# Kernel optimization log

Measured on AMD Instinct MI355X. Metric: run time of the kernel, lower is better.

The kernel has to match this reference:

```python
import jax, jax.numpy as jnp
import numpy as np


def _gcn_conv(x, edge_index, W, b):
    # PyG GCNConv: h = x @ W; out = D^{-1/2}(A+I)D^{-1/2} h + b
    N = x.shape[0]
    src, dst = edge_index[0], edge_index[1]
    # degree with self-loops (edge weights = 1)
    deg = jax.ops.segment_sum(jnp.ones(src.shape[0], x.dtype), dst, num_segments=N) + 1.0
    dis = jax.lax.rsqrt(deg)  # deg >= 1 so finite
    h = x @ W  # [N, F_out]
    norm = dis[src] * dis[dst]  # [E]
    msg = h[src] * norm[:, None]  # [E, F_out] -- dominant memory traffic
    agg = jax.ops.segment_sum(msg, dst, num_segments=N)
    # self-loop contribution: norm_ii = dis_i^2
    out = agg + h * (dis * dis)[:, None] + b
    return out


def setup_inputs() -> dict:
    key = jax.random.key(0)
    k1, k2, k3, k4, k5, k6 = jax.random.split(key, 6)
    N, E = 100000, 1600000
    in_ch, hid, out_ch = 256, 128, 64  # hid = 2*out_channels
    x = jax.random.normal(k1, (N, in_ch), dtype=jnp.float32)
    edge_index = jax.random.randint(k2, (2, E), 0, N, dtype=jnp.int64)
    # Glorot-style init for GCN weights, zero bias (PyG default)
    W1 = jax.random.normal(k3, (in_ch, hid), dtype=jnp.float32) / np.sqrt(in_ch)
    b1 = jnp.zeros((hid,), jnp.float32)
    W2 = jax.random.normal(k4, (hid, out_ch), dtype=jnp.float32) / np.sqrt(hid)
    b2 = jnp.zeros((out_ch,), jnp.float32)
    return {"x": x, "edge_index": edge_index, "W1": W1, "b1": b1, "W2": W2, "b2": b2}


def reference(x, edge_index, W1, b1, W2, b2):
    # Encoder.forward: k=2 layers of activation(GCNConv(x, edge_index))
    h = jax.nn.relu(_gcn_conv(x, edge_index, W1, b1))
    h = jax.nn.relu(_gcn_conv(h, edge_index, W2, b2))
    return h
```

## Files before the change

kernel.cpp:

```cpp
#include <hip/hip_runtime.h>
#include <math.h>

#define THREADS 256

static inline int cdiv(long long a, long long b) { return (int)((a + b - 1) / b); }

typedef __attribute__((ext_vector_type(8))) short bf16x8;
typedef __attribute__((ext_vector_type(4))) float f32x4;

__device__ inline unsigned f2bf_rne_u(float f) {
    unsigned u = __builtin_bit_cast(unsigned, f);
    return (u + 0x7FFFu + ((u >> 16) & 1u)) >> 16;
}
__device__ inline float bfu2f(unsigned h) {
    unsigned u = h << 16;
    return __builtin_bit_cast(float, u);
}


__global__ __launch_bounds__(THREADS)
void hist_rank_kernel(const int* __restrict__ dst, int* __restrict__ deg,
                      int* __restrict__ rank, int E) {
    int i = blockIdx.x * blockDim.x + threadIdx.x;
    if (i < E) rank[i] = atomicAdd(&deg[dst[i]], 1);
}


#define SCAN_BLOCK 256
#define SCAN_ITEMS 4

__global__ __launch_bounds__(SCAN_BLOCK)
void scan_block_kernel(const int* __restrict__ in, int* __restrict__ out,
                       int* __restrict__ blockSums, float* __restrict__ dis, int n) {
    __shared__ int sdata[SCAN_BLOCK];
    int base = blockIdx.x * (SCAN_BLOCK * SCAN_ITEMS);
    int tid = threadIdx.x;
    int v[SCAN_ITEMS];
    int sum = 0;
    #pragma unroll
    for (int k = 0; k < SCAN_ITEMS; ++k) {
        int idx = base + tid * SCAN_ITEMS + k;
        v[k] = (idx < n) ? in[idx] : 0;
        if (idx < n) dis[idx] = rsqrtf((float)v[k] + 1.0f);
        sum += v[k];
    }
    sdata[tid] = sum;
    __syncthreads();
    for (int off = 1; off < SCAN_BLOCK; off <<= 1) {
        int t = (tid >= off) ? sdata[tid - off] : 0;
        __syncthreads();
        sdata[tid] += t;
        __syncthreads();
    }
    if (tid == SCAN_BLOCK - 1) blockSums[blockIdx.x] = sdata[SCAN_BLOCK - 1];
    int run = (tid == 0) ? 0 : sdata[tid - 1];
    #pragma unroll
    for (int k = 0; k < SCAN_ITEMS; ++k) {
        int idx = base + tid * SCAN_ITEMS + k;
        if (idx < n) out[idx] = run;
        run += v[k];
    }
}

__global__ __launch_bounds__(SCAN_BLOCK)
void scan_sums_kernel(int* __restrict__ blockSums, int nB) {
    __shared__ int sdata[SCAN_BLOCK];
    int tid = threadIdx.x;
    sdata[tid] = (tid < nB) ? blockSums[tid] : 0;
    __syncthreads();
    for (int off = 1; off < SCAN_BLOCK; off <<= 1) {
        int t = (tid >= off) ? sdata[tid - off] : 0;
        __syncthreads();
        sdata[tid] += t;
        __syncthreads();
    }
    int excl = (tid == 0) ? 0 : sdata[tid - 1];
    if (tid < nB) blockSums[tid] = excl;
}

__global__ __launch_bounds__(SCAN_BLOCK)
void scan_add_kernel(int* __restrict__ out, const int* __restrict__ blockSums,
                     int n, int E) {
    int base = blockIdx.x * (SCAN_BLOCK * SCAN_ITEMS);
    int add = blockSums[blockIdx.x];
    #pragma unroll
    for (int k = 0; k < SCAN_ITEMS; ++k) {
        int idx = base + threadIdx.x * SCAN_ITEMS + k;
        if (idx < n) out[idx] += add;
    }
    if (blockIdx.x == 0 && threadIdx.x == 0) out[n] = E;
}


__global__ __launch_bounds__(THREADS)
void fill_col_rank_kernel(const int* __restrict__ src, const int* __restrict__ dst,
                          const int* __restrict__ rank, const int* __restrict__ rowptr,
                          int* __restrict__ col, int E) {
    int base = (blockIdx.x * blockDim.x + threadIdx.x) * 4;
    if (base + 3 < E) {
        int4 d = *(const int4*)(dst + base);
        int4 r = *(const int4*)(rank + base);
        int4 s = *(const int4*)(src + base);
        col[rowptr[d.x] + r.x] = s.x;
        col[rowptr[d.y] + r.y] = s.y;
        col[rowptr[d.z] + r.z] = s.z;
        col[rowptr[d.w] + r.w] = s.w;
    } else {
        for (int e = base; e < E; ++e)
            col[rowptr[dst[e]] + rank[e]] = src[e];
    }
}


template<int F, int VEC>
__global__ __launch_bounds__(THREADS)
void gather_bf16_kernel(const unsigned short* __restrict__ g, const int* __restrict__ col,
                        const int* __restrict__ rowptr, const float* __restrict__ dis,
                        const float* __restrict__ bias, float* __restrict__ out, int N) {
    int wid = (int)((blockIdx.x * (long long)blockDim.x + threadIdx.x) >> 6);
    wid = __builtin_amdgcn_readfirstlane(wid);
    const int lane = threadIdx.x & 63;
    if (wid >= N) return;
    const float di = dis[wid];
    const int loff = lane * VEC;

    float acc0 = 0.0f, acc1 = 0.0f;

    auto loadrow = [&](int s) -> unsigned {
        const unsigned short* p = g + (size_t)s * F + loff;
        if (VEC == 2) return *(const unsigned*)p;
        else return (unsigned)*p;
    };
    auto addconv = [&](unsigned u) {
        if (VEC == 2) {
            acc0 += bfu2f(u & 0xFFFFu);
            acc1 += __builtin_bit_cast(float, u & 0xFFFF0000u);
        } else {
            acc0 += bfu2f(u);
        }
    };

    addconv(loadrow(wid));

    int start = __builtin_amdgcn_readfirstlane(rowptr[wid]);
    int end   = __builtin_amdgcn_readfirstlane(rowptr[wid + 1]);
    const int* c = col + start;
    int rem = end - start;

    if (rem >= 4) {
        int s0 = __builtin_amdgcn_readfirstlane(c[0]);
        int s1 = __builtin_amdgcn_readfirstlane(c[1]);
        int s2 = __builtin_amdgcn_readfirstlane(c[2]);
        int s3 = __builtin_amdgcn_readfirstlane(c[3]);
        unsigned u0 = loadrow(s0), u1 = loadrow(s1), u2 = loadrow(s2), u3 = loadrow(s3);
        c += 4; rem -= 4;
        while (rem >= 4) {
            int t0 = __builtin_amdgcn_readfirstlane(c[0]);
            int t1 = __builtin_amdgcn_readfirstlane(c[1]);
            int t2 = __builtin_amdgcn_readfirstlane(c[2]);
            int t3 = __builtin_amdgcn_readfirstlane(c[3]);
            unsigned v0 = loadrow(t0), v1 = loadrow(t1), v2 = loadrow(t2), v3 = loadrow(t3);
            addconv(u0); addconv(u1); addconv(u2); addconv(u3);
            u0 = v0; u1 = v1; u2 = v2; u3 = v3;
            c += 4; rem -= 4;
        }
        addconv(u0); addconv(u1); addconv(u2); addconv(u3);
    }
    while (rem > 0) {
        int s = __builtin_amdgcn_readfirstlane(c[0]);
        addconv(loadrow(s));
        ++c; --rem;
    }

    float* orow = out + (size_t)wid * F + loff;
    float v0 = di * acc0 + bias[loff];
    if (VEC == 2) {
        float v1 = di * acc1 + bias[loff + 1];
        float2 st = make_float2(fmaxf(v0, 0.0f), fmaxf(v1, 0.0f));
        *(float2*)orow = st;
    } else {
        *orow = fmaxf(v0, 0.0f);
    }
}


__global__ __launch_bounds__(64)
void make_bfrag_both_kernel(const float* __restrict__ W1, short* __restrict__ f1,
                            const float* __restrict__ W2, short* __restrict__ f2) {
    int lane = threadIdx.x;
    int b = blockIdx.x;
    const float* W; short* frag; int NCT, ctks;
    if (b < 64) { W = W1; frag = f1; NCT = 8; ctks = b; }
    else        { W = W2; frag = f2; NCT = 4; ctks = b - 64; }
    int Nn = NCT * 16;
    int ct = ctks % NCT;
    int ks = ctks / NCT;
    int colc = ct * 16 + (lane & 15);
    int kbase = ks * 32 + (lane >> 4) * 8;
    short* base = frag + (size_t)ctks * 1024 + lane * 8;
    #pragma unroll
    for (int j = 0; j < 8; ++j) {
        float v = W[(size_t)(kbase + j) * Nn + colc];
        unsigned h = f2bf_rne_u(v);
        base[j] = (short)h;
        base[512 + j] = (short)f2bf_rne_u(v - bfu2f(h));
    }
}

template<int NCT, int KS>
__global__ __launch_bounds__(THREADS)
void mfma_gemm_bf16out_kernel(const float* __restrict__ A, const short* __restrict__ Bfrag,
                              unsigned short* __restrict__ G, const float* __restrict__ dis,
                              int M) {
    constexpr int K = KS * 32;
    constexpr int Nn = NCT * 16;
    const int lane = threadIdx.x & 63;
    const int wave = threadIdx.x >> 6;
    const int rowBase = blockIdx.x * 128 + wave * 32;
    const int arow0 = rowBase + (lane & 15);
    const int kgrp = (lane >> 4) * 8;

    f32x4 acc[2][NCT] = {};

    for (int ks = 0; ks < KS; ++ks) {
        const int kbase = ks * 32 + kgrp;
        bf16x8 ahi[2], alo[2];
        #pragma unroll
        for (int t = 0; t < 2; ++t) {
            int r = arow0 + t * 16;
            if (r >= M) r = M - 1;
            const float* ap = A + (size_t)r * K + kbase;
            float4 v0 = *(const float4*)ap;
            float4 v1 = *(const float4*)(ap + 4);
            float av[8] = {v0.x, v0.y, v0.z, v0.w, v1.x, v1.y, v1.z, v1.w};
            #pragma unroll
            for (int j = 0; j < 8; ++j) {
                unsigned h = f2bf_rne_u(av[j]);
                ahi[t][j] = (short)h;
                alo[t][j] = (short)f2bf_rne_u(av[j] - bfu2f(h));
            }
        }
        #pragma unroll
        for (int ct = 0; ct < NCT; ++ct) {
            const short* bp = Bfrag + (size_t)(ks * NCT + ct) * 1024 + lane * 8;
            bf16x8 bhi = *(const bf16x8*)bp;
            bf16x8 blo = *(const bf16x8*)(bp + 512);
            #pragma unroll
            for (int t = 0; t < 2; ++t) {
                acc[t][ct] = __builtin_amdgcn_mfma_f32_16x16x32_bf16(ahi[t], bhi, acc[t][ct], 0, 0, 0);
                acc[t][ct] = __builtin_amdgcn_mfma_f32_16x16x32_bf16(ahi[t], blo, acc[t][ct], 0, 0, 0);
                acc[t][ct] = __builtin_amdgcn_mfma_f32_16x16x32_bf16(alo[t], bhi, acc[t][ct], 0, 0, 0);
            }
        }
    }

    const int drow0 = rowBase + (lane >> 4) * 4;
    #pragma unroll
    for (int t = 0; t < 2; ++t) {
        #pragma unroll
        for (int r = 0; r < 4; ++r) {
            int row = drow0 + t * 16 + r;
            if (row < M) {
                float dval = dis[row];
                unsigned short* gp = G + (size_t)row * Nn + (lane & 15);
                #pragma unroll
                for (int ct = 0; ct < NCT; ++ct)
                    gp[ct * 16] = (unsigned short)f2bf_rne_u(acc[t][ct][r] * dval);
            }
        }
    }
}


#define BM 64
#define BN 64
#define BK 16

__global__ __launch_bounds__(THREADS)
void sgemm_kernel(const float* __restrict__ A, const float* __restrict__ B,
                  float* __restrict__ C, int M, int N, int K) {
    __shared__ float As[BK][BM + 1];
    __shared__ float Bs[BK][BN + 1];

    const int tid = threadIdx.x;
    const int tr = tid / 16;
    const int tc = tid % 16;
    const int rowBase = blockIdx.y * BM;
    const int colBase = blockIdx.x * BN;

    float acc[4][4] = {};

    for (int k0 = 0; k0 < K; k0 += BK) {
        #pragma unroll
        for (int i = tid; i < BM * BK; i += THREADS) {
            int r = i / BK, c = i % BK;
            int gr = rowBase + r;
            As[c][r] = (gr < M) ? A[(size_t)gr * K + k0 + c] : 0.0f;
        }
        #pragma unroll
        for (int i = tid; i < BK * BN; i += THREADS) {
            int r = i / BN, c = i % BN;
            Bs[r][c] = B[(size_t)(k0 + r) * N + colBase + c];
        }
        __syncthreads();

        #pragma unroll
        for (int k = 0; k < BK; ++k) {
            float a[4], b[4];
            #pragma unroll
            for (int m = 0; m < 4; ++m) a[m] = As[k][tr * 4 + m];
            #pragma unroll
            for (int n = 0; n < 4; ++n) b[n] = Bs[k][tc * 4 + n];
            #pragma unroll
            for (int m = 0; m < 4; ++m)
                #pragma unroll
                for (int n = 0; n < 4; ++n)
                    acc[m][n] += a[m] * b[n];
        }
        __syncthreads();
    }

    #pragma unroll
    for (int m = 0; m < 4; ++m) {
        int gr = rowBase + tr * 4 + m;
        if (gr >= M) continue;
        #pragma unroll
        for (int n = 0; n < 4; ++n) {
            C[(size_t)gr * N + colBase + tc * 4 + n] = acc[m][n];
        }
    }
}

__global__ __launch_bounds__(THREADS)
void init_agg_kernel(const float* __restrict__ h, const float* __restrict__ dis,
                     float* __restrict__ agg, int N, int F) {
    int i = blockIdx.x * blockDim.x + threadIdx.x;
    int total = N * (F / 4);
    if (i >= total) return;
    int node = i / (F / 4);
    float d = dis[node];
    float w = d * d;
    float4 v = ((const float4*)h)[i];
    v.x *= w; v.y *= w; v.z *= w; v.w *= w;
    ((float4*)agg)[i] = v;
}

__global__ __launch_bounds__(THREADS)
void edge_scatter_kernel(const float* __restrict__ h, const int* __restrict__ src,
                         const int* __restrict__ dst, const float* __restrict__ dis,
                         float* __restrict__ agg, int E, int F) {
    int lanesPerEdge = F / 4;
    int tid = blockIdx.x * blockDim.x + threadIdx.x;
    int e = tid / lanesPerEdge;
    int c = tid % lanesPerEdge;
    if (e >= E) return;
    int s = src[e];
    int d = dst[e];
    float w = dis[s] * dis[d];
    float4 hv = ((const float4*)(h + (size_t)s * F))[c];
    float* ap = agg + (size_t)d * F + (size_t)c * 4;
    atomicAdd(ap + 0, hv.x * w);
    atomicAdd(ap + 1, hv.y * w);
    atomicAdd(ap + 2, hv.z * w);
    atomicAdd(ap + 3, hv.w * w);
}

__global__ __launch_bounds__(THREADS)
void finalize_kernel(const float* __restrict__ agg, const float* __restrict__ b,
                     float* __restrict__ out, int N, int F) {
    int i = blockIdx.x * blockDim.x + threadIdx.x;
    int total = N * (F / 4);
    if (i >= total) return;
    int c4 = i % (F / 4);
    float4 bv = ((const float4*)b)[c4];
    float4 v = ((const float4*)agg)[i];
    v.x = fmaxf(v.x + bv.x, 0.0f);
    v.y = fmaxf(v.y + bv.y, 0.0f);
    v.z = fmaxf(v.z + bv.z, 0.0f);
    v.w = fmaxf(v.w + bv.w, 0.0f);
    ((float4*)out)[i] = v;
}

__global__ __launch_bounds__(THREADS)
void fdeg_kernel(const int* __restrict__ dst, float* __restrict__ deg, int E) {
    int i = blockIdx.x * blockDim.x + threadIdx.x;
    if (i < E) atomicAdd(&deg[dst[i]], 1.0f);
}

__global__ __launch_bounds__(THREADS)
void fdis_kernel(float* __restrict__ deg, int N) {
    int i = blockIdx.x * blockDim.x + threadIdx.x;
    if (i < N) deg[i] = rsqrtf(deg[i] + 1.0f);
}


extern "C" void kernel_launch(void* const* d_in, const int* in_sizes, int n_in,
                              void* d_out, int out_size, void* d_ws, size_t ws_size,
                              hipStream_t stream) {
    const float* x  = (const float*)d_in[0];
    const int*   ei = (const int*)d_in[1];
    const float* W1 = (const float*)d_in[2];
    const float* b1 = (const float*)d_in[3];
    const float* W2 = (const float*)d_in[4];
    const float* b2 = (const float*)d_in[5];

    const int E    = in_sizes[1] / 2;
    const int hid  = in_sizes[3];
    const int outc = in_sizes[5];
    const int inc  = in_sizes[2] / hid;
    const int N    = in_sizes[0] / inc;

    const int* src = ei;
    const int* dst = ei + E;
    float* out = (float*)d_out;
    char* ws = (char*)d_ws;

    auto al = [](size_t v) { return (v + 255) & ~(size_t)255; };
    size_t o_dis  = 0;
    size_t o_deg  = al(o_dis + (size_t)N * 4);
    size_t o_rp   = al(o_deg + (size_t)N * 4);
    size_t o_bs   = al(o_rp + ((size_t)N + 1) * 4);
    size_t o_col  = al(o_bs + 4096);
    size_t o_rank = al(o_col + (size_t)E * 4);
    size_t o_bf1  = al(o_rank + (size_t)E * 4);
    size_t o_bf2  = al(o_bf1 + 131072);
    size_t o_G    = al(o_bf2 + 32768);
    size_t o_B    = al(o_G + (size_t)N * hid * 2);
    size_t need   = o_B + (size_t)N * hid * 4;

    if (ws_size >= need && N <= SCAN_BLOCK * SCAN_BLOCK * SCAN_ITEMS &&
        hid == 128 && outc == 64 && inc == 256) {
        float* dis    = (float*)(ws + o_dis);
        int*   deg    = (int*)(ws + o_deg);
        int*   rowptr = (int*)(ws + o_rp);
        int*   bsums  = (int*)(ws + o_bs);
        int*   col    = (int*)(ws + o_col);
        int*   rank   = (int*)(ws + o_rank);
        short* bf1    = (short*)(ws + o_bf1);
        short* bf2    = (short*)(ws + o_bf2);
        unsigned short* gbuf = (unsigned short*)(ws + o_G);
        float* out1   = (float*)(ws + o_B);

        hipMemsetAsync(deg, 0, (size_t)N * 4, stream);
        hist_rank_kernel<<<cdiv(E, THREADS), THREADS, 0, stream>>>(dst, deg, rank, E);

        int nB = cdiv(N, SCAN_BLOCK * SCAN_ITEMS);
        scan_block_kernel<<<nB, SCAN_BLOCK, 0, stream>>>(deg, rowptr, bsums, dis, N);
        scan_sums_kernel<<<1, SCAN_BLOCK, 0, stream>>>(bsums, nB);
        scan_add_kernel<<<nB, SCAN_BLOCK, 0, stream>>>(rowptr, bsums, N, E);

        fill_col_rank_kernel<<<cdiv(cdiv(E, 4), THREADS), THREADS, 0, stream>>>(
            src, dst, rank, rowptr, col, E);

        make_bfrag_both_kernel<<<80, 64, 0, stream>>>(W1, bf1, W2, bf2);

        mfma_gemm_bf16out_kernel<8, 8><<<cdiv(N, 128), THREADS, 0, stream>>>(x, bf1, gbuf, dis, N);
        gather_bf16_kernel<128, 2><<<cdiv((long long)N * 64, THREADS), THREADS, 0, stream>>>(
            gbuf, col, rowptr, dis, b1, out1, N);

        mfma_gemm_bf16out_kernel<4, 4><<<cdiv(N, 128), THREADS, 0, stream>>>(out1, bf2, gbuf, dis, N);
        gather_bf16_kernel<64, 1><<<cdiv((long long)N * 64, THREADS), THREADS, 0, stream>>>(
            gbuf, col, rowptr, dis, b2, out, N);
        return;
    }

    float* dis = (float*)ws;
    size_t off1 = ((size_t)N * 4 + 255) & ~(size_t)255;
    float* h1 = (float*)(ws + off1);
    size_t off2 = off1 + ((((size_t)N * hid * 4) + 255) & ~(size_t)255);
    float* agg1 = (float*)(ws + off2);
    float* h2   = agg1;
    float* agg2 = agg1 + (size_t)N * outc;

    hipMemsetAsync(dis, 0, (size_t)N * 4, stream);
    fdeg_kernel<<<cdiv(E, THREADS), THREADS, 0, stream>>>(dst, dis, E);
    fdis_kernel<<<cdiv(N, THREADS), THREADS, 0, stream>>>(dis, N);

    {
        dim3 grid(hid / BN, cdiv(N, BM));
        sgemm_kernel<<<grid, THREADS, 0, stream>>>(x, W1, h1, N, hid, inc);
    }
    init_agg_kernel<<<cdiv((long long)N * hid / 4, THREADS), THREADS, 0, stream>>>(h1, dis, agg1, N, hid);
    edge_scatter_kernel<<<cdiv((long long)E * (hid / 4), THREADS), THREADS, 0, stream>>>(
        h1, src, dst, dis, agg1, E, hid);
    finalize_kernel<<<cdiv((long long)N * hid / 4, THREADS), THREADS, 0, stream>>>(agg1, b1, h1, N, hid);

    {
        dim3 grid(outc / BN, cdiv(N, BM));
        sgemm_kernel<<<grid, THREADS, 0, stream>>>(h1, W2, h2, N, outc, hid);
    }
    init_agg_kernel<<<cdiv((long long)N * outc / 4, THREADS), THREADS, 0, stream>>>(h2, dis, agg2, N, outc);
    edge_scatter_kernel<<<cdiv((long long)E * (outc / 4), THREADS), THREADS, 0, stream>>>(
        h2, src, dst, dis, agg2, E, outc);
    finalize_kernel<<<cdiv((long long)N * outc / 4, THREADS), THREADS, 0, stream>>>(agg2, b2, out, N, outc);
}
```

Baseline: 279.3 us.

## Merge independent CSR-build and GEMM launches into combined block-partitioned kernels

Independent stages now share launches, with blocks split by index. The degree histogram runs alongside building the weight fragments, and the CSR column fill runs alongside the first-layer MFMA GEMM. This cuts two kernel launches and lets the scatter-bound fill overlap with the compute-bound GEMM. The histogram now handles four edges per thread using vectorized int4 loads and stores. The risks are uneven block mixes within one grid and the GEMM's register pressure applying to the fill blocks.

```diff
diff --git a/kernel.cpp b/kernel.cpp
--- a/kernel.cpp
+++ b/kernel.cpp
@@ -18,11 +18,155 @@
 }
 
 
-__global__ __launch_bounds__(THREADS)
-void hist_rank_kernel(const int* __restrict__ dst, int* __restrict__ deg,
-                      int* __restrict__ rank, int E) {
-    int i = blockIdx.x * blockDim.x + threadIdx.x;
-    if (i < E) rank[i] = atomicAdd(&deg[dst[i]], 1);
+__device__ __forceinline__ void hist_body(const int* __restrict__ dst, int* __restrict__ deg,
+                                          int* __restrict__ rank, int E, int blk) {
+    int base = (blk * THREADS + (int)threadIdx.x) * 4;
+    if (base + 3 < E) {
+        int4 d = *(const int4*)(dst + base);
+        int4 r;
+        r.x = atomicAdd(&deg[d.x], 1);
+        r.y = atomicAdd(&deg[d.y], 1);
+        r.z = atomicAdd(&deg[d.z], 1);
+        r.w = atomicAdd(&deg[d.w], 1);
+        *(int4*)(rank + base) = r;
+    } else {
+        for (int e = base; e < E; ++e) rank[e] = atomicAdd(&deg[dst[e]], 1);
+    }
+}
+
+__device__ __forceinline__ void bfrag_unit(const float* __restrict__ W, short* __restrict__ frag,
+                                           int NCT, int ctks, int lane) {
+    int Nn = NCT * 16;
+    int ct = ctks % NCT;
+    int ks = ctks / NCT;
+    int colc = ct * 16 + (lane & 15);
+    int kbase = ks * 32 + (lane >> 4) * 8;
+    short* base = frag + (size_t)ctks * 1024 + lane * 8;
+    #pragma unroll
+    for (int j = 0; j < 8; ++j) {
+        float v = W[(size_t)(kbase + j) * Nn + colc];
+        unsigned h = f2bf_rne_u(v);
+        base[j] = (short)h;
+        base[512 + j] = (short)f2bf_rne_u(v - bfu2f(h));
+    }
+}
+
+__device__ __forceinline__ void fill_body(const int* __restrict__ src, const int* __restrict__ dst,
+                                          const int* __restrict__ rank, const int* __restrict__ rowptr,
+                                          int* __restrict__ col, int E, int blk) {
+    int base = (blk * THREADS + (int)threadIdx.x) * 4;
+    if (base + 3 < E) {
+        int4 d = *(const int4*)(dst + base);
+        int4 r = *(const int4*)(rank + base);
+        int4 s = *(const int4*)(src + base);
+        col[rowptr[d.x] + r.x] = s.x;
+        col[rowptr[d.y] + r.y] = s.y;
+        col[rowptr[d.z] + r.z] = s.z;
+        col[rowptr[d.w] + r.w] = s.w;
+    } else {
+        for (int e = base; e < E; ++e)
+            col[rowptr[dst[e]] + rank[e]] = src[e];
+    }
+}
+
+template<int NCT, int KS>
+__device__ __forceinline__ void gemm_body(const float* __restrict__ A, const short* __restrict__ Bfrag,
+                                          unsigned short* __restrict__ G, const float* __restrict__ dis,
+                                          int M, int blk) {
+    constexpr int K = KS * 32;
+    constexpr int Nn = NCT * 16;
+    const int lane = threadIdx.x & 63;
+    const int wave = threadIdx.x >> 6;
+    const int rowBase = blk * 128 + wave * 32;
+    const int arow0 = rowBase + (lane & 15);
+    const int kgrp = (lane >> 4) * 8;
+
+    f32x4 acc[2][NCT] = {};
+
+    for (int ks = 0; ks < KS; ++ks) {
+        const int kbase = ks * 32 + kgrp;
+        bf16x8 ahi[2], alo[2];
+        #pragma unroll
+        for (int t = 0; t < 2; ++t) {
+            int r = arow0 + t * 16;
+            if (r >= M) r = M - 1;
+            const float* ap = A + (size_t)r * K + kbase;
+            float4 v0 = *(const float4*)ap;
+            float4 v1 = *(const float4*)(ap + 4);
+            float av[8] = {v0.x, v0.y, v0.z, v0.w, v1.x, v1.y, v1.z, v1.w};
+            #pragma unroll
+            for (int j = 0; j < 8; ++j) {
+                unsigned h = f2bf_rne_u(av[j]);
+                ahi[t][j] = (short)h;
+                alo[t][j] = (short)f2bf_rne_u(av[j] - bfu2f(h));
+            }
+        }
+        #pragma unroll
+        for (int ct = 0; ct < NCT; ++ct) {
+            const short* bp = Bfrag + (size_t)(ks * NCT + ct) * 1024 + lane * 8;
+            bf16x8 bhi = *(const bf16x8*)bp;
+            bf16x8 blo = *(const bf16x8*)(bp + 512);
+            #pragma unroll
+            for (int t = 0; t < 2; ++t) {
+                acc[t][ct] = __builtin_amdgcn_mfma_f32_16x16x32_bf16(ahi[t], bhi, acc[t][ct], 0, 0, 0);
+                acc[t][ct] = __builtin_amdgcn_mfma_f32_16x16x32_bf16(ahi[t], blo, acc[t][ct], 0, 0, 0);
+                acc[t][ct] = __builtin_amdgcn_mfma_f32_16x16x32_bf16(alo[t], bhi, acc[t][ct], 0, 0, 0);
+            }
+        }
+    }
+
+    const int drow0 = rowBase + (lane >> 4) * 4;
+    #pragma unroll
+    for (int t = 0; t < 2; ++t) {
+        #pragma unroll
+        for (int r = 0; r < 4; ++r) {
+            int row = drow0 + t * 16 + r;
+            if (row < M) {
+                float dval = dis[row];
+                unsigned short* gp = G + (size_t)row * Nn + (lane & 15);
+                #pragma unroll
+                for (int ct = 0; ct < NCT; ++ct)
+                    gp[ct * 16] = (unsigned short)f2bf_rne_u(acc[t][ct][r] * dval);
+            }
+        }
+    }
+}
+
+
+__global__ __launch_bounds__(THREADS)
+void hist_bfrag_kernel(const int* __restrict__ dst, int* __restrict__ deg, int* __restrict__ rank, int E,
+                       const float* __restrict__ W1, short* __restrict__ bf1,
+                       const float* __restrict__ W2, short* __restrict__ bf2, int nbHist) {
+    int b = (int)blockIdx.x;
+    if (b < nbHist) {
+        hist_body(dst, deg, rank, E, b);
+    } else {
+        int u = (b - nbHist) * 4 + ((int)threadIdx.x >> 6);
+        int lane = threadIdx.x & 63;
+        if (u < 64) bfrag_unit(W1, bf1, 8, u, lane);
+        else if (u < 80) bfrag_unit(W2, bf2, 4, u - 64, lane);
+    }
+}
+
+template<int NCT, int KS>
+__global__ __launch_bounds__(THREADS)
+void fill_gemm_kernel(const int* __restrict__ src, const int* __restrict__ dst,
+                      const int* __restrict__ rank, const int* __restrict__ rowptr,
+                      int* __restrict__ col, int E,
+                      const float* __restrict__ A, const short* __restrict__ Bfrag,
+                      unsigned short* __restrict__ G, const float* __restrict__ dis,
+                      int M, int nbFill) {
+    int b = (int)blockIdx.x;
+    if (b < nbFill) fill_body(src, dst, rank, rowptr, col, E, b);
+    else gemm_body<NCT, KS>(A, Bfrag, G, dis, M, b - nbFill);
+}
+
+template<int NCT, int KS>
+__global__ __launch_bounds__(THREADS)
+void mfma_gemm_bf16out_kernel(const float* __restrict__ A, const short* __restrict__ Bfrag,
+                              unsigned short* __restrict__ G, const float* __restrict__ dis,
+                              int M) {
+    gemm_body<NCT, KS>(A, Bfrag, G, dis, M, (int)blockIdx.x);
 }
 
 
@@ -89,26 +233,6 @@
         if (idx < n) out[idx] += add;
     }
     if (blockIdx.x == 0 && threadIdx.x == 0) out[n] = E;
-}
-
-
-__global__ __launch_bounds__(THREADS)
-void fill_col_rank_kernel(const int* __restrict__ src, const int* __restrict__ dst,
-                          const int* __restrict__ rank, const int* __restrict__ rowptr,
-                          int* __restrict__ col, int E) {
-    int base = (blockIdx.x * blockDim.x + threadIdx.x) * 4;
-    if (base + 3 < E) {
-        int4 d = *(const int4*)(dst + base);
-        int4 r = *(const int4*)(rank + base);
-        int4 s = *(const int4*)(src + base);
-        col[rowptr[d.x] + r.x] = s.x;
-        col[rowptr[d.y] + r.y] = s.y;
-        col[rowptr[d.z] + r.z] = s.z;
-        col[rowptr[d.w] + r.w] = s.w;
-    } else {
-        for (int e = base; e < E; ++e)
-            col[rowptr[dst[e]] + rank[e]] = src[e];
-    }
 }
 
 
@@ -180,94 +304,6 @@
         *(float2*)orow = st;
     } else {
         *orow = fmaxf(v0, 0.0f);
-    }
-}
-
-
-__global__ __launch_bounds__(64)
-void make_bfrag_both_kernel(const float* __restrict__ W1, short* __restrict__ f1,
-                            const float* __restrict__ W2, short* __restrict__ f2) {
-    int lane = threadIdx.x;
-    int b = blockIdx.x;
-    const float* W; short* frag; int NCT, ctks;
-    if (b < 64) { W = W1; frag = f1; NCT = 8; ctks = b; }
-    else        { W = W2; frag = f2; NCT = 4; ctks = b - 64; }
-    int Nn = NCT * 16;
-    int ct = ctks % NCT;
-    int ks = ctks / NCT;
-    int colc = ct * 16 + (lane & 15);
-    int kbase = ks * 32 + (lane >> 4) * 8;
-    short* base = frag + (size_t)ctks * 1024 + lane * 8;
-    #pragma unroll
-    for (int j = 0; j < 8; ++j) {
-        float v = W[(size_t)(kbase + j) * Nn + colc];
-        unsigned h = f2bf_rne_u(v);
-        base[j] = (short)h;
-        base[512 + j] = (short)f2bf_rne_u(v - bfu2f(h));
-    }
-}
-
-template<int NCT, int KS>
-__global__ __launch_bounds__(THREADS)
-void mfma_gemm_bf16out_kernel(const float* __restrict__ A, const short* __restrict__ Bfrag,
-                              unsigned short* __restrict__ G, const float* __restrict__ dis,
-                              int M) {
-    constexpr int K = KS * 32;
-    constexpr int Nn = NCT * 16;
-    const int lane = threadIdx.x & 63;
-    const int wave = threadIdx.x >> 6;
-    const int rowBase = blockIdx.x * 128 + wave * 32;
-    const int arow0 = rowBase + (lane & 15);
-    const int kgrp = (lane >> 4) * 8;
-
-    f32x4 acc[2][NCT] = {};
-
-    for (int ks = 0; ks < KS; ++ks) {
-        const int kbase = ks * 32 + kgrp;
-        bf16x8 ahi[2], alo[2];
-        #pragma unroll
-        for (int t = 0; t < 2; ++t) {
-            int r = arow0 + t * 16;
-            if (r >= M) r = M - 1;
-            const float* ap = A + (size_t)r * K + kbase;
-            float4 v0 = *(const float4*)ap;
-            float4 v1 = *(const float4*)(ap + 4);
-            float av[8] = {v0.x, v0.y, v0.z, v0.w, v1.x, v1.y, v1.z, v1.w};
-            #pragma unroll
-            for (int j = 0; j < 8; ++j) {
-                unsigned h = f2bf_rne_u(av[j]);
-                ahi[t][j] = (short)h;
-                alo[t][j] = (short)f2bf_rne_u(av[j] - bfu2f(h));
-            }
-        }
-        #pragma unroll
-        for (int ct = 0; ct < NCT; ++ct) {
-            const short* bp = Bfrag + (size_t)(ks * NCT + ct) * 1024 + lane * 8;
-            bf16x8 bhi = *(const bf16x8*)bp;
-            bf16x8 blo = *(const bf16x8*)(bp + 512);
-            #pragma unroll
-            for (int t = 0; t < 2; ++t) {
-                acc[t][ct] = __builtin_amdgcn_mfma_f32_16x16x32_bf16(ahi[t], bhi, acc[t][ct], 0, 0, 0);
-                acc[t][ct] = __builtin_amdgcn_mfma_f32_16x16x32_bf16(ahi[t], blo, acc[t][ct], 0, 0, 0);
-                acc[t][ct] = __builtin_amdgcn_mfma_f32_16x16x32_bf16(alo[t], bhi, acc[t][ct], 0, 0, 0);
-            }
-        }
-    }
-
-    const int drow0 = rowBase + (lane >> 4) * 4;
-    #pragma unroll
-    for (int t = 0; t < 2; ++t) {
-        #pragma unroll
-        for (int r = 0; r < 4; ++r) {
-            int row = drow0 + t * 16 + r;
-            if (row < M) {
-                float dval = dis[row];
-                unsigned short* gp = G + (size_t)row * Nn + (lane & 15);
-                #pragma unroll
-                for (int ct = 0; ct < NCT; ++ct)
-                    gp[ct * 16] = (unsigned short)f2bf_rne_u(acc[t][ct][r] * dval);
-            }
-        }
     }
 }
 
@@ -441,20 +477,22 @@
         unsigned short* gbuf = (unsigned short*)(ws + o_G);
         float* out1   = (float*)(ws + o_B);
 
+        const int nbHist = cdiv(E, 4 * THREADS);
+        const int nbFill = cdiv(E, 4 * THREADS);
+        const int nbGemm1 = cdiv(N, 128);
+
         hipMemsetAsync(deg, 0, (size_t)N * 4, stream);
-        hist_rank_kernel<<<cdiv(E, THREADS), THREADS, 0, stream>>>(dst, deg, rank, E);
+        hist_bfrag_kernel<<<nbHist + 20, THREADS, 0, stream>>>(
+            dst, deg, rank, E, W1, bf1, W2, bf2, nbHist);
 
         int nB = cdiv(N, SCAN_BLOCK * SCAN_ITEMS);
         scan_block_kernel<<<nB, SCAN_BLOCK, 0, stream>>>(deg, rowptr, bsums, dis, N);
         scan_sums_kernel<<<1, SCAN_BLOCK, 0, stream>>>(bsums, nB);
         scan_add_kernel<<<nB, SCAN_BLOCK, 0, stream>>>(rowptr, bsums, N, E);
 
-        fill_col_rank_kernel<<<cdiv(cdiv(E, 4), THREADS), THREADS, 0, stream>>>(
-            src, dst, rank, rowptr, col, E);
-
-        make_bfrag_both_kernel<<<80, 64, 0, stream>>>(W1, bf1, W2, bf2);
-
-        mfma_gemm_bf16out_kernel<8, 8><<<cdiv(N, 128), THREADS, 0, stream>>>(x, bf1, gbuf, dis, N);
+        fill_gemm_kernel<8, 8><<<nbFill + nbGemm1, THREADS, 0, stream>>>(
+            src, dst, rank, rowptr, col, E, x, bf1, gbuf, dis, N, nbFill);
+
         gather_bf16_kernel<128, 2><<<cdiv((long long)N * 64, THREADS), THREADS, 0, stream>>>(
             gbuf, col, rowptr, dis, b1, out1, N);
 
```

Result: no change. 274.0 us (-1.9%).
